# Optimization experiments

Measured on AMD Instinct MI355X. Metric: run time of the kernel, lower is better.

## Reference

```python
import jax, jax.numpy as jnp
import numpy as np

N_FFT = 128
HOP = 32            # fft_stride
WIN_LEN = 512       # window_length
STRIDE = 128        # MPF stride
FS = 2000.0
BANDS = [(0.0, 100.0), (100.0, 200.0), (200.0, 300.0), (300.0, 500.0), (500.0, 750.0), (750.0, 1000.0)]
FRAME_SIZE = WIN_LEN // HOP   # 16 STFT frames per MPF window
FRAME_STEP = STRIDE // HOP    # 4


def _freq_masks():
    freqs = np.fft.rfftfreq(N_FFT, d=1.0 / FS)  # (F,) Hz
    m = np.stack([(freqs > lo) & (freqs <= hi) for lo, hi in BANDS]).astype(np.float32)  # (K, F)
    return jnp.asarray(m)


def setup_inputs() -> dict:
    key = jax.random.key(0)
    return {"inputs": jax.random.normal(key, (8, 16, 32768), dtype=jnp.float32)}


def reference(inputs) -> jnp.ndarray:
    # inputs: (B, C, T)
    B, C, T = inputs.shape
    window = jnp.hanning(N_FFT).astype(inputs.dtype)  # symmetric hann == torch periodic=False
    wnorm = jnp.linalg.norm(window)

    # --- channelwise STFT (center=False, onesided) ---
    n_frames = 1 + (T - N_FFT) // HOP
    fidx = np.arange(n_frames)[:, None] * HOP + np.arange(N_FFT)[None, :]  # (n_frames, N_FFT)
    frames = inputs[..., fidx] * window                                    # (B, C, n_frames, N_FFT)
    stft = jnp.fft.rfft(frames, axis=-1) / wnorm                           # (B, C, n_frames, F) complex

    # --- unfold STFT frames into MPF windows ---
    n_win = (n_frames - FRAME_SIZE) // FRAME_STEP + 1
    widx = np.arange(n_win)[:, None] * FRAME_STEP + np.arange(FRAME_SIZE)  # (n_win, FRAME_SIZE)
    X = stft[:, :, widx, :]                       # (B, C, n_win, FRAME_SIZE, F)
    X = jnp.transpose(X, (0, 2, 4, 1, 3))         # (B, W, F, C, S)

    # --- cross-spectral density, squared magnitude ---
    csd = jnp.einsum('bwfcs,bwfds->bwfcd', X, X.conj()) / FRAME_SIZE  # (B, W, F, C, C) complex
    P = jnp.abs(csd) ** 2                                             # real (B, W, F, C, C)

    # --- frequency-band averaging ---
    masks = _freq_masks()                                             # (K, F)
    band = jnp.einsum('bwfcd,kf->bwkcd', P, masks) / masks.sum(axis=1)[:, None, None]

    # --- SPD matrix log via eigh ---
    evals, evecs = jnp.linalg.eigh(band)                              # (B,W,K,C), (B,W,K,C,C)
    logv = jnp.nan_to_num(jnp.log(evals), nan=0.0, neginf=0.0)
    out = jnp.einsum('...ie,...e,...je->...ij', evecs, logv, evecs)   # (B, W, K, C, C)

    # time-last layout: (B, K, C, C, W)
    return jnp.transpose(out, (0, 2, 3, 4, 1))
```

## Files before the change

### kernel.cpp

```cpp
#include <hip/hip_runtime.h>
#include <math.h>

#define T_LEN 32768
#define NCH   16
#define NB    8
#define NWIN  252
#define NBAND 6
#define NPAIR 136

typedef float v2f __attribute__((ext_vector_type(2)));

struct PairTab { int c[NPAIR]; int d[NPAIR]; };
constexpr PairTab mkpairs() {
    PairTab P{}; int p = 0;
    for (int c = 0; c < 16; ++c)
        for (int d = c; d < 16; ++d) { P.c[p] = c; P.d[p] = d; ++p; }
    return P;
}
constexpr PairTab PT = mkpairs();

template<int G>
__device__ __forceinline__ void acc_csd(const v2f* __restrict__ X,
                                        v2f* __restrict__ acc)
{
#pragma unroll
    for (int t = 0; t < 17; ++t) {
        const int c = PT.c[G + 8 * t];
        const int d = PT.d[G + 8 * t];
        v2f Xc = X[c], Xd = X[d];
        acc[t] = __builtin_elementwise_fma(Xc, Xd.xx, acc[t]);
        acc[t] = __builtin_elementwise_fma((v2f){Xc.y, -Xc.x}, Xd.yy, acc[t]);
    }
}

#define SWZ(v, imm)  __int_as_float(__builtin_amdgcn_ds_swizzle(__float_as_int(v), (imm)))
#define DPPQ(v, ctl) __int_as_float(__builtin_amdgcn_mov_dpp(__float_as_int(v), (ctl), 0xF, 0xF, true))

__device__ __forceinline__ void bfv(v2f& v, v2f p, v2f tw, v2f twn, v2f sg)
{
    v2f t = __builtin_elementwise_fma(sg, v, p);
    v = __builtin_elementwise_fma(t.xx, tw, t.yy * twn);
}
#define BF2(v, EX, TW, TWN, SG) \
    { v2f p_; p_.x = EX(v.x); p_.y = EX(v.y); bfv(v, p_, TW, TWN, SG); }

__global__ __launch_bounds__(512, 2) void csd_band_kernel(const float* __restrict__ x,
                                                          float* __restrict__ band)
{
    const int w    = blockIdx.x;
    const int b    = blockIdx.y;
    const int tid  = threadIdx.x;
    const int lane = tid & 63;
    const int g    = tid >> 6;
    const int f    = lane + 1;

    __shared__ v2f  X2[NCH][64];
    __shared__ v2f  scr[8][2][64];
    __shared__ float bl[NBAND][NPAIR];
    __shared__ unsigned char pc_[NPAIR], pd_[NPAIR];

    for (int i = tid; i < NBAND * NPAIR; i += 512) (&bl[0][0])[i] = 0.f;
    if (tid < NPAIR) {
        int rem = tid, c = 0;
        while (rem >= 16 - c) { rem -= 16 - c; ++c; }
        pc_[tid] = (unsigned char)c; pd_[tid] = (unsigned char)(c + rem);
    }

    const double PI = 3.14159265358979323846;
    const float  WI = (float)(1.0 / sqrt(47.625));
    const float wlo = (float)(0.5 - 0.5 * cos(2.0 * PI * (double)lane / 127.0)) * WI;
    const float whi = (float)(0.5 - 0.5 * cos(2.0 * PI * (double)(lane + 64) / 127.0)) * WI;

    const float PIF = 3.14159265358979f;
    float w128r, w128i;
    { float a = -2.f * PIF * (float)lane / 128.f; sincosf(a, &w128i, &w128r); }
    float t32r, t32i, t16r, t16i, t8r, t8i, t4r, t4i, t2r, t2i;
    { float a = (lane & 32) ? -2.f * PIF * (float)(lane & 31) / 64.f : 0.f; sincosf(a, &t32i, &t32r); }
    { float a = (lane & 16) ? -2.f * PIF * (float)(lane & 15) / 32.f : 0.f; sincosf(a, &t16i, &t16r); }
    { float a = (lane &  8) ? -2.f * PIF * (float)(lane &  7) / 16.f : 0.f; sincosf(a, &t8i,  &t8r ); }
    { float a = (lane &  4) ? -2.f * PIF * (float)(lane &  3) /  8.f : 0.f; sincosf(a, &t4i,  &t4r ); }
    { float a = (lane &  2) ? -2.f * PIF * (float)(lane &  1) /  4.f : 0.f; sincosf(a, &t2i,  &t2r ); }
    const v2f TWH  = { w128r,  w128i }, TWHN = { -w128i, w128r };
    const v2f TW32 = { t32r, t32i },    TW32N = { -t32i, t32r };
    const v2f TW16 = { t16r, t16i },    TW16N = { -t16i, t16r };
    const v2f TW8  = { t8r,  t8i  },    TW8N  = { -t8i,  t8r  };
    const v2f TW4  = { t4r,  t4i  },    TW4N  = { -t4i,  t4r  };
    const v2f TW2  = { t2r,  t2i  },    TW2N  = { -t2i,  t2r  };
    const v2f SG32 = { (lane & 32) ? -1.f : 1.f, (lane & 32) ? -1.f : 1.f };
    const v2f SG16 = { (lane & 16) ? -1.f : 1.f, (lane & 16) ? -1.f : 1.f };
    const v2f SG8  = { (lane &  8) ? -1.f : 1.f, (lane &  8) ? -1.f : 1.f };
    const v2f SG4  = { (lane &  4) ? -1.f : 1.f, (lane &  4) ? -1.f : 1.f };
    const v2f SG2  = { (lane &  2) ? -1.f : 1.f, (lane &  2) ? -1.f : 1.f };
    const v2f SG1  = { (lane &  1) ? -1.f : 1.f, (lane &  1) ? -1.f : 1.f };

    const int bp32 = 4 * (lane ^ 32);
    const int La = (int)(__brev((unsigned)(f >> 1)) >> 26);
    const int Lb = (int)(__brev((unsigned)((128 - f) >> 1)) >> 26);
    const int pa = f & 1;

    v2f acc[17];
#pragma unroll
    for (int t = 0; t < 17; ++t) acc[t] = (v2f){0.f, 0.f};

    const float* xp0 = x + (size_t)(b * NCH + g) * T_LEN + (size_t)w * 128;
    const float* xp1 = xp0 + 8 * (size_t)T_LEN;

    __syncthreads();

    for (int s = 0; s < 16; ++s) {
        v2f S0 = (v2f){ xp0[s * 32 + lane],      xp1[s * 32 + lane]      } * wlo;
        v2f S1 = (v2f){ xp0[s * 32 + lane + 64], xp1[s * 32 + lane + 64] } * whi;

        {
            v2f D = S0 - S1;
            S0 = S0 + S1;
            S1 = __builtin_elementwise_fma(D.xx, TWH, D.yy * TWHN);
        }
#define EX32(v) __int_as_float(__builtin_amdgcn_ds_bpermute(bp32, __float_as_int(v)))
#define EX16(v) SWZ(v, 0x401F)
#define EX8(v)  SWZ(v, 0x201F)
#define EX4(v)  SWZ(v, 0x101F)
#define EX2(v)  DPPQ(v, 0x4E)
#define EX1(v)  DPPQ(v, 0xB1)
        BF2(S0, EX32, TW32, TW32N, SG32)
        BF2(S1, EX32, TW32, TW32N, SG32)
        BF2(S0, EX16, TW16, TW16N, SG16)
        BF2(S1, EX16, TW16, TW16N, SG16)
        BF2(S0, EX8,  TW8,  TW8N,  SG8)
        BF2(S1, EX8,  TW8,  TW8N,  SG8)
        BF2(S0, EX4,  TW4,  TW4N,  SG4)
        BF2(S1, EX4,  TW4,  TW4N,  SG4)
        BF2(S0, EX2,  TW2,  TW2N,  SG2)
        BF2(S1, EX2,  TW2,  TW2N,  SG2)
        {
            v2f p_; p_.x = EX1(S0.x); p_.y = EX1(S0.y);
            S0 = __builtin_elementwise_fma(SG1, S0, p_);
        }
        {
            v2f p_; p_.x = EX1(S1.x); p_.y = EX1(S1.y);
            S1 = __builtin_elementwise_fma(SG1, S1, p_);
        }

        scr[g][0][lane] = S0;
        scr[g][1][lane] = S1;
        v2f Ua = scr[g][pa][La];
        v2f Ub = scr[g][pa][Lb];
        v2f X0 = { 0.5f * (Ua.x + Ub.x), 0.5f * (Ua.y - Ub.y) };
        v2f X1 = { 0.5f * (Ua.y + Ub.y), 0.5f * (Ub.x - Ua.x) };

        __syncthreads();
        X2[g][lane]     = X0;
        X2[g + 8][lane] = X1;
        __syncthreads();

        v2f X[16];
#pragma unroll
        for (int c = 0; c < 16; ++c) X[c] = X2[c][lane];
        switch (g) {
            case 0: acc_csd<0>(X, acc); break;
            case 1: acc_csd<1>(X, acc); break;
            case 2: acc_csd<2>(X, acc); break;
            case 3: acc_csd<3>(X, acc); break;
            case 4: acc_csd<4>(X, acc); break;
            case 5: acc_csd<5>(X, acc); break;
            case 6: acc_csd<6>(X, acc); break;
            default: acc_csd<7>(X, acc); break;
        }
    }

    const int kband = (lane < 6) ? 0 : (lane < 12) ? 1 : (lane < 19) ? 2
                    : (lane < 32) ? 3 : (lane < 48) ? 4 : 5;
#pragma unroll
    for (int t = 0; t < 17; ++t) {
        float vv = fmaf(acc[t].x, acc[t].x, acc[t].y * acc[t].y);
        atomicAdd(&bl[kband][g + 8 * t], vv);
    }
    __syncthreads();

    const float rs[NBAND] = { 1.f/(256.f*6.f), 1.f/(256.f*6.f), 1.f/(256.f*7.f),
                              1.f/(256.f*13.f), 1.f/(256.f*16.f), 1.f/(256.f*16.f) };
    float* bb = band + (size_t)(b * NWIN + w) * (NBAND * 256);
    for (int i = tid; i < NBAND * NPAIR; i += 512) {
        int k = i / NPAIR, p = i - k * NPAIR;
        int c = pc_[p], d = pd_[p];
        float val = bl[k][p] * rs[k];
        bb[k * 256 + c * 16 + d] = val;
        bb[k * 256 + d * 16 + c] = val;
    }
}

__device__ __forceinline__ void tourney(int rr, int j, int& p, int& q)
{
    if (j == 0) { p = 15; q = rr; }
    else { p = (rr + j) % 15; q = (rr + 15 - j) % 15; }
    if (p > q) { int t_ = p; p = q; q = t_; }
}

__global__ __launch_bounds__(512) void eig_log_kernel(const float* __restrict__ band,
                                                      float* __restrict__ out)
{
    const int tid  = threadIdx.x;
    const int g    = tid >> 6;
    const int lane = tid & 63;
    const int m    = blockIdx.x * 8 + g;
    const int k    = m % NBAND;
    const int bw   = m / NBAND;
    const int w    = bw % NWIN;
    const int b    = bw / NWIN;
    const int j    = lane >> 3;
    const int n2   = lane & 7;

    __shared__ float A[8][16][18];
    __shared__ float DT[8][16][18];
    __shared__ float VT[8][16][18];
    __shared__ float lv[8][16];

    const float* M = band + ((size_t)(b * NWIN + w) * NBAND + k) * 256;
#pragma unroll
    for (int it = 0; it < 4; ++it) {
        int i = lane + it * 64, r = i >> 4, c = i & 15;
        A[g][r][c]  = M[i];
        VT[g][r][c] = (r == c) ? 1.f : 0.f;
    }

    for (int sweep = 0; sweep < 4; ++sweep) {
        for (int rr = 0; rr < 15; ++rr) {
            int p, q; tourney(rr, j, p, q);
            float app = A[g][p][p], aqq = A[g][q][q], apq = A[g][p][q];
            float c_ = 1.f, s_ = 0.f;
            if (apq != 0.f) {
                float tau = (aqq - app) / (2.f * apq);
                float t   = copysignf(1.f, tau) / (fabsf(tau) + sqrtf(1.f + tau * tau));
                c_ = 1.f / sqrtf(1.f + t * t);
                s_ = t * c_;
            }
            float2 ap = *(const float2*)&A[g][p][2 * n2];
            float2 aq = *(const float2*)&A[g][q][2 * n2];
            DT[g][2 * n2][p]     = c_ * ap.x - s_ * aq.x;
            DT[g][2 * n2 + 1][p] = c_ * ap.y - s_ * aq.y;
            DT[g][2 * n2][q]     = s_ * ap.x + c_ * aq.x;
            DT[g][2 * n2 + 1][q] = s_ * ap.y + c_ * aq.y;

            float2 dp = *(const float2*)&DT[g][p][2 * n2];
            float2 dq = *(const float2*)&DT[g][q][2 * n2];
            *(float2*)&A[g][p][2 * n2] = make_float2(c_ * dp.x - s_ * dq.x,
                                                     c_ * dp.y - s_ * dq.y);
            *(float2*)&A[g][q][2 * n2] = make_float2(s_ * dp.x + c_ * dq.x,
                                                     s_ * dp.y + c_ * dq.y);
            float2 vp = *(const float2*)&VT[g][p][2 * n2];
            float2 vq = *(const float2*)&VT[g][q][2 * n2];
            *(float2*)&VT[g][p][2 * n2] = make_float2(c_ * vp.x - s_ * vq.x,
                                                      c_ * vp.y - s_ * vq.y);
            *(float2*)&VT[g][q][2 * n2] = make_float2(s_ * vp.x + c_ * vq.x,
                                                      s_ * vp.y + c_ * vq.y);
        }
    }

    if (lane < 16) {
        float l = logf(A[g][lane][lane]);
        if (isnan(l) || isinf(l)) l = 0.f;
        lv[g][lane] = l;
    }

    float* ob = out + (size_t)(b * NBAND + k) * 256 * NWIN;
#pragma unroll
    for (int it = 0; it < 4; ++it) {
        int i = lane + it * 64, c = i >> 4, d = i & 15;
        float sum = 0.f;
#pragma unroll
        for (int e = 0; e < 16; ++e) sum = fmaf(VT[g][e][c] * lv[g][e], VT[g][e][d], sum);
        ob[(size_t)i * NWIN + w] = sum;
    }
}

extern "C" void kernel_launch(void* const* d_in, const int* in_sizes, int n_in,
                              void* d_out, int out_size, void* d_ws, size_t ws_size,
                              hipStream_t stream)
{
    const float* x    = (const float*)d_in[0];
    float*       out  = (float*)d_out;
    float*       band = (float*)d_ws;

    dim3 g1(NWIN, NB), b1(512);
    hipLaunchKernelGGL(csd_band_kernel, g1, b1, 0, stream, x, band);

    dim3 g2(NB * NWIN * NBAND / 8), b2(512);
    hipLaunchKernelGGL(eig_log_kernel, g2, b2, 0, stream, band, out);
}
```

Measured before the change: 361.7 us.

## Process two STFT frames per iteration and swizzle FFT scratch indices

The frame loop now handles two STFT frames per iteration, so the FFT butterflies for both frames are interleaved and the two block-wide barriers are paid once per pair of frames instead of once per frame. The scratch buffer used for the real-FFT post-processing gets an XOR swizzle on its indices to reduce LDS bank conflicts on the bit-reversed reads. In exchange, shared memory doubles for the scratch and X2 buffers and the loop body holds more live registers, which under launch_bounds(512,2) may cause spills.

Result: slower. 391.5 us (+8.2%).

```diff
diff --git a/kernel.cpp b/kernel.cpp
--- a/kernel.cpp
+++ b/kernel.cpp
@@ -44,6 +44,8 @@
 #define BF2(v, EX, TW, TWN, SG) \
     { v2f p_; p_.x = EX(v.x); p_.y = EX(v.y); bfv(v, p_, TW, TWN, SG); }
 
+#define SCRIDX(i) ((i) ^ (((i) >> 3) & 7))
+
 __global__ __launch_bounds__(512, 2) void csd_band_kernel(const float* __restrict__ x,
                                                           float* __restrict__ band)
 {
@@ -54,8 +56,8 @@
     const int g    = tid >> 6;
     const int f    = lane + 1;
 
-    __shared__ v2f  X2[NCH][64];
-    __shared__ v2f  scr[8][2][64];
+    __shared__ v2f  X2[2][NCH][64];
+    __shared__ v2f  scr[8][4][64];
     __shared__ float bl[NBAND][NPAIR];
     __shared__ unsigned char pc_[NPAIR], pd_[NPAIR];
 
@@ -94,9 +96,10 @@
     const v2f SG1  = { (lane &  1) ? -1.f : 1.f, (lane &  1) ? -1.f : 1.f };
 
     const int bp32 = 4 * (lane ^ 32);
-    const int La = (int)(__brev((unsigned)(f >> 1)) >> 26);
-    const int Lb = (int)(__brev((unsigned)((128 - f) >> 1)) >> 26);
+    const int La = SCRIDX((int)(__brev((unsigned)(f >> 1)) >> 26));
+    const int Lb = SCRIDX((int)(__brev((unsigned)((128 - f) >> 1)) >> 26));
     const int pa = f & 1;
+    const int sw = SCRIDX(lane);
 
     v2f acc[17];
 #pragma unroll
@@ -107,14 +110,23 @@
 
     __syncthreads();
 
-    for (int s = 0; s < 16; ++s) {
-        v2f S0 = (v2f){ xp0[s * 32 + lane],      xp1[s * 32 + lane]      } * wlo;
-        v2f S1 = (v2f){ xp0[s * 32 + lane + 64], xp1[s * 32 + lane + 64] } * whi;
-
-        {
-            v2f D = S0 - S1;
-            S0 = S0 + S1;
-            S1 = __builtin_elementwise_fma(D.xx, TWH, D.yy * TWHN);
+#pragma unroll 1
+    for (int it = 0; it < 8; ++it) {
+        const int sA = 2 * it;
+        v2f A0 = (v2f){ xp0[sA * 32 + lane],       xp1[sA * 32 + lane]       } * wlo;
+        v2f A1 = (v2f){ xp0[sA * 32 + lane + 64],  xp1[sA * 32 + lane + 64]  } * whi;
+        v2f B0 = (v2f){ xp0[sA * 32 + lane + 32],  xp1[sA * 32 + lane + 32]  } * wlo;
+        v2f B1 = (v2f){ xp0[sA * 32 + lane + 96],  xp1[sA * 32 + lane + 96]  } * whi;
+
+        {
+            v2f D = A0 - A1;
+            A0 = A0 + A1;
+            A1 = __builtin_elementwise_fma(D.xx, TWH, D.yy * TWHN);
+        }
+        {
+            v2f D = B0 - B1;
+            B0 = B0 + B1;
+            B1 = __builtin_elementwise_fma(D.xx, TWH, D.yy * TWHN);
         }
 #define EX32(v) __int_as_float(__builtin_amdgcn_ds_bpermute(bp32, __float_as_int(v)))
 #define EX16(v) SWZ(v, 0x401F)
@@ -122,49 +134,76 @@
 #define EX4(v)  SWZ(v, 0x101F)
 #define EX2(v)  DPPQ(v, 0x4E)
 #define EX1(v)  DPPQ(v, 0xB1)
-        BF2(S0, EX32, TW32, TW32N, SG32)
-        BF2(S1, EX32, TW32, TW32N, SG32)
-        BF2(S0, EX16, TW16, TW16N, SG16)
-        BF2(S1, EX16, TW16, TW16N, SG16)
-        BF2(S0, EX8,  TW8,  TW8N,  SG8)
-        BF2(S1, EX8,  TW8,  TW8N,  SG8)
-        BF2(S0, EX4,  TW4,  TW4N,  SG4)
-        BF2(S1, EX4,  TW4,  TW4N,  SG4)
-        BF2(S0, EX2,  TW2,  TW2N,  SG2)
-        BF2(S1, EX2,  TW2,  TW2N,  SG2)
-        {
-            v2f p_; p_.x = EX1(S0.x); p_.y = EX1(S0.y);
-            S0 = __builtin_elementwise_fma(SG1, S0, p_);
-        }
-        {
-            v2f p_; p_.x = EX1(S1.x); p_.y = EX1(S1.y);
-            S1 = __builtin_elementwise_fma(SG1, S1, p_);
-        }
-
-        scr[g][0][lane] = S0;
-        scr[g][1][lane] = S1;
-        v2f Ua = scr[g][pa][La];
-        v2f Ub = scr[g][pa][Lb];
-        v2f X0 = { 0.5f * (Ua.x + Ub.x), 0.5f * (Ua.y - Ub.y) };
-        v2f X1 = { 0.5f * (Ua.y + Ub.y), 0.5f * (Ub.x - Ua.x) };
+        BF2(A0, EX32, TW32, TW32N, SG32)
+        BF2(A1, EX32, TW32, TW32N, SG32)
+        BF2(B0, EX32, TW32, TW32N, SG32)
+        BF2(B1, EX32, TW32, TW32N, SG32)
+        BF2(A0, EX16, TW16, TW16N, SG16)
+        BF2(A1, EX16, TW16, TW16N, SG16)
+        BF2(B0, EX16, TW16, TW16N, SG16)
+        BF2(B1, EX16, TW16, TW16N, SG16)
+        BF2(A0, EX8,  TW8,  TW8N,  SG8)
+        BF2(A1, EX8,  TW8,  TW8N,  SG8)
+        BF2(B0, EX8,  TW8,  TW8N,  SG8)
+        BF2(B1, EX8,  TW8,  TW8N,  SG8)
+        BF2(A0, EX4,  TW4,  TW4N,  SG4)
+        BF2(A1, EX4,  TW4,  TW4N,  SG4)
+        BF2(B0, EX4,  TW4,  TW4N,  SG4)
+        BF2(B1, EX4,  TW4,  TW4N,  SG4)
+        BF2(A0, EX2,  TW2,  TW2N,  SG2)
+        BF2(A1, EX2,  TW2,  TW2N,  SG2)
+        BF2(B0, EX2,  TW2,  TW2N,  SG2)
+        BF2(B1, EX2,  TW2,  TW2N,  SG2)
+        {
+            v2f p_; p_.x = EX1(A0.x); p_.y = EX1(A0.y);
+            A0 = __builtin_elementwise_fma(SG1, A0, p_);
+        }
+        {
+            v2f p_; p_.x = EX1(A1.x); p_.y = EX1(A1.y);
+            A1 = __builtin_elementwise_fma(SG1, A1, p_);
+        }
+        {
+            v2f p_; p_.x = EX1(B0.x); p_.y = EX1(B0.y);
+            B0 = __builtin_elementwise_fma(SG1, B0, p_);
+        }
+        {
+            v2f p_; p_.x = EX1(B1.x); p_.y = EX1(B1.y);
+            B1 = __builtin_elementwise_fma(SG1, B1, p_);
+        }
+
+        scr[g][0][sw] = A0;
+        scr[g][1][sw] = A1;
+        scr[g][2][sw] = B0;
+        scr[g][3][sw] = B1;
+        v2f UaA = scr[g][pa][La],     UbA = scr[g][pa][Lb];
+        v2f UaB = scr[g][2 + pa][La], UbB = scr[g][2 + pa][Lb];
+        v2f XA0 = { 0.5f * (UaA.x + UbA.x), 0.5f * (UaA.y - UbA.y) };
+        v2f XA1 = { 0.5f * (UaA.y + UbA.y), 0.5f * (UbA.x - UaA.x) };
+        v2f XB0 = { 0.5f * (UaB.x + UbB.x), 0.5f * (UaB.y - UbB.y) };
+        v2f XB1 = { 0.5f * (UaB.y + UbB.y), 0.5f * (UbB.x - UaB.x) };
 
         __syncthreads();
-        X2[g][lane]     = X0;
-        X2[g + 8][lane] = X1;
+        X2[0][g][lane]     = XA0;
+        X2[0][g + 8][lane] = XA1;
+        X2[1][g][lane]     = XB0;
+        X2[1][g + 8][lane] = XB1;
         __syncthreads();
 
-        v2f X[16];
-#pragma unroll
-        for (int c = 0; c < 16; ++c) X[c] = X2[c][lane];
-        switch (g) {
-            case 0: acc_csd<0>(X, acc); break;
-            case 1: acc_csd<1>(X, acc); break;
-            case 2: acc_csd<2>(X, acc); break;
-            case 3: acc_csd<3>(X, acc); break;
-            case 4: acc_csd<4>(X, acc); break;
-            case 5: acc_csd<5>(X, acc); break;
-            case 6: acc_csd<6>(X, acc); break;
-            default: acc_csd<7>(X, acc); break;
+#pragma unroll
+        for (int fr = 0; fr < 2; ++fr) {
+            v2f X[16];
+#pragma unroll
+            for (int c = 0; c < 16; ++c) X[c] = X2[fr][c][lane];
+            switch (g) {
+                case 0: acc_csd<0>(X, acc); break;
+                case 1: acc_csd<1>(X, acc); break;
+                case 2: acc_csd<2>(X, acc); break;
+                case 3: acc_csd<3>(X, acc); break;
+                case 4: acc_csd<4>(X, acc); break;
+                case 5: acc_csd<5>(X, acc); break;
+                case 6: acc_csd<6>(X, acc); break;
+                default: acc_csd<7>(X, acc); break;
+            }
         }
     }
 
```

## Double-buffer input frames via global_load_lds and use DPP for stride-8 exchange

Applied to the files above, without the earlier changes.

The per-step global loads of the 16 input frames are replaced with asynchronous global-to-LDS loads into a double-buffered staging array, so the next frame is prefetched while the current one is transformed. Explicit vmcnt waits gate consumption. The stride-8 butterfly exchange switches from ds_swizzle to a DPP row-shift-style control, and __syncthreads is replaced with an lgkmcnt wait plus s_barrier. This adds LDS usage and relies on hand-placed waitcnts and on the DPP control having the intended lane-exchange semantics, which risks correctness.

Result: no change. 367.0 us (+1.5%).

```diff
diff --git a/kernel.cpp b/kernel.cpp
--- a/kernel.cpp
+++ b/kernel.cpp
@@ -44,6 +44,16 @@
 #define BF2(v, EX, TW, TWN, SG) \
     { v2f p_; p_.x = EX(v.x); p_.y = EX(v.y); bfv(v, p_, TW, TWN, SG); }
 
+typedef const __attribute__((address_space(1))) void gas_void;
+typedef __attribute__((address_space(3))) void las_void;
+#define GLD(gp, lp) __builtin_amdgcn_global_load_lds((gas_void*)(gp), (las_void*)(lp), 4, 0, 0)
+
+__device__ __forceinline__ void barrier_lgkm()
+{
+    asm volatile("s_waitcnt lgkmcnt(0)" ::: "memory");
+    __builtin_amdgcn_s_barrier();
+}
+
 __global__ __launch_bounds__(512, 2) void csd_band_kernel(const float* __restrict__ x,
                                                           float* __restrict__ band)
 {
@@ -54,8 +64,9 @@
     const int g    = tid >> 6;
     const int f    = lane + 1;
 
-    __shared__ v2f  X2[NCH][64];
-    __shared__ v2f  scr[8][2][64];
+    __shared__ v2f   X2[NCH][64];
+    __shared__ v2f   scr[8][2][64];
+    __shared__ float stage[2][8][256];
     __shared__ float bl[NBAND][NPAIR];
     __shared__ unsigned char pc_[NPAIR], pd_[NPAIR];
 
@@ -105,11 +116,33 @@
     const float* xp0 = x + (size_t)(b * NCH + g) * T_LEN + (size_t)w * 128;
     const float* xp1 = xp0 + 8 * (size_t)T_LEN;
 
-    __syncthreads();
+    {
+        float* l0 = &stage[0][g][0];
+        GLD(xp0 + lane,      l0);
+        GLD(xp0 + 64 + lane, l0 + 64);
+        GLD(xp1 + lane,      l0 + 128);
+        GLD(xp1 + 64 + lane, l0 + 192);
+    }
+
+    barrier_lgkm();
 
     for (int s = 0; s < 16; ++s) {
-        v2f S0 = (v2f){ xp0[s * 32 + lane],      xp1[s * 32 + lane]      } * wlo;
-        v2f S1 = (v2f){ xp0[s * 32 + lane + 64], xp1[s * 32 + lane + 64] } * whi;
+        const int cur = s & 1;
+        if (s < 15) {
+            float* l0 = &stage[cur ^ 1][g][0];
+            const float* g0 = xp0 + (s + 1) * 32;
+            const float* g1 = xp1 + (s + 1) * 32;
+            GLD(g0 + lane,      l0);
+            GLD(g0 + 64 + lane, l0 + 64);
+            GLD(g1 + lane,      l0 + 128);
+            GLD(g1 + 64 + lane, l0 + 192);
+            asm volatile("s_waitcnt vmcnt(4)" ::: "memory");
+        } else {
+            asm volatile("s_waitcnt vmcnt(0)" ::: "memory");
+        }
+
+        v2f S0 = (v2f){ stage[cur][g][lane],      stage[cur][g][128 + lane] } * wlo;
+        v2f S1 = (v2f){ stage[cur][g][64 + lane], stage[cur][g][192 + lane] } * whi;
 
         {
             v2f D = S0 - S1;
@@ -118,7 +151,7 @@
         }
 #define EX32(v) __int_as_float(__builtin_amdgcn_ds_bpermute(bp32, __float_as_int(v)))
 #define EX16(v) SWZ(v, 0x401F)
-#define EX8(v)  SWZ(v, 0x201F)
+#define EX8(v)  DPPQ(v, 0x128)
 #define EX4(v)  SWZ(v, 0x101F)
 #define EX2(v)  DPPQ(v, 0x4E)
 #define EX1(v)  DPPQ(v, 0xB1)
@@ -148,10 +181,10 @@
         v2f X0 = { 0.5f * (Ua.x + Ub.x), 0.5f * (Ua.y - Ub.y) };
         v2f X1 = { 0.5f * (Ua.y + Ub.y), 0.5f * (Ub.x - Ua.x) };
 
-        __syncthreads();
+        barrier_lgkm();
         X2[g][lane]     = X0;
         X2[g + 8][lane] = X1;
-        __syncthreads();
+        barrier_lgkm();
 
         v2f X[16];
 #pragma unroll
```
